# Kernel tuning notes

Hardware: AMD Instinct MI355X
Metric: run time of the kernel (lower is better)

The kernel has to match this reference:

```python
import jax, jax.numpy as jnp
import numpy as np

N_STEPS = 20
ALPHA, BETA = 0.9, 0.8  # synaptic / membrane decay (unused given zero carried state, kept for clarity)


def _lcn_spiking_layer(h, knn, w, b):
    """h: [N, d_in]; knn: [d_out, K] indices into d_in; w: [d_out, K]; b: [1, d_out].
    Gather K neighbors per output node, weight, reduce, then snntorch Synaptic
    update with zero carried state (the source never stores returned syn/mem):
      syn = ALPHA*0 + I = I ; reset = (prev_mem > thr) = 0 ; mem = BETA*0 + syn - 0 = I
    and the layer output is mem (the source keeps the 3rd return value)."""
    g = h[:, knn]                                  # [N, d_out, K] irregular gather
    cur = jnp.sum(g * w[None, :, :], axis=2) + b   # [N, d_out]
    syn = ALPHA * jnp.zeros_like(cur) + cur
    mem = BETA * jnp.zeros_like(cur) + syn         # reset term is zero
    return mem


def setup_inputs() -> dict:
    key = jax.random.key(0)
    B, T, IN_DIM, K, OUT = 32, N_STEPS, 14400, 25, 2
    dims = [7200, 3600, 1800, 900, 450]
    ks = jax.random.split(key, 13)
    inp = {"x": jax.random.normal(ks[0], (B, T, IN_DIM), dtype=jnp.float32)}
    prev = IN_DIM
    for i, d in enumerate(dims):
        inp[f"w{i}"] = jax.random.normal(ks[1 + i], (d, K), dtype=jnp.float32) * (2.0 / K) ** 0.5
        inp[f"b{i}"] = jnp.zeros((1, d), dtype=jnp.float32)
        inp[f"knn{i}"] = jax.random.randint(ks[6 + i], (d, K), 0, prev)
        prev = d
    inp["Wfc"] = jax.random.normal(ks[11], (dims[-1], OUT), dtype=jnp.float32) * (1.0 / dims[-1]) ** 0.5
    inp["bfc"] = jnp.zeros((OUT,), dtype=jnp.float32)
    return inp


def reference(x, w0, w1, w2, w3, w4, b0, b1, b2, b3, b4, Wfc, bfc,
              knn0, knn1, knn2, knn3, knn4):
    # Source loops over 20 timesteps with independent (state never carried) work;
    # fold time into batch to vectorize, then keep the last step's angle only,
    # exactly matching the returned value of the torch forward.
    B, T, D = x.shape
    h = x.reshape(B * T, D)
    layers = ((w0, b0, knn0), (w1, b1, knn1), (w2, b2, knn2), (w3, b3, knn3), (w4, b4, knn4))
    for w, b, knn in layers:
        h = _lcn_spiking_layer(h, knn, w, b)
    angle = h @ Wfc + bfc                     # [B*T, out_dim]
    angle = angle.reshape(B, T, -1)[:, -1]    # last timestep, as in the source
    return angle
```

## Files before the change

kernel.cpp:

```cpp
#include <hip/hip_runtime.h>
#include <hip/hip_bf16.h>


#define ROWS 32
#define TSTEPS 20
#define D0 14400
#define D1 7200
#define D2 3600
#define D3 1800
#define D4 900
#define D5 450
#define KNB 25

template <int DIN, int DOUT, int JPB>
__global__ __launch_bounds__(256)
void layer_lds(const float* __restrict__ hin_base, long long row_stride,
               float* __restrict__ hout,
               const float* __restrict__ w, const float* __restrict__ bvec,
               const int* __restrict__ knn)
{
    __shared__ float s[DIN];
    const int row = blockIdx.y;
    const float* hin = hin_base + (long long)row * row_stride;

    const float4* src = reinterpret_cast<const float4*>(hin);
    float4* dst = reinterpret_cast<float4*>(s);
#pragma unroll 1
    for (int i = threadIdx.x; i < DIN / 4; i += 256)
        dst[i] = src[i];
    __syncthreads();

    const int j0 = blockIdx.x * JPB;
#pragma unroll 1
    for (int j = j0 + threadIdx.x; j < j0 + JPB; j += 256) {
        const int*   kn = knn + j * KNB;
        const float* ww = w   + j * KNB;
        float acc = bvec[j];
#pragma unroll
        for (int k = 0; k < KNB; ++k)
            acc += s[kn[k]] * ww[k];
        hout[row * DOUT + j] = acc;
    }
}

__global__ __launch_bounds__(256)
void lcn_l4_fc(const float* __restrict__ h4,
               const float* __restrict__ w4, const float* __restrict__ b4, const int* __restrict__ knn4,
               const float* __restrict__ Wfc, const float* __restrict__ bfc,
               float* __restrict__ out)
{
    __shared__ float s4[D4];
    __shared__ float s5[D5];

    const int row = blockIdx.x;
    const float* hrow = h4 + row * D4;
    for (int i = threadIdx.x; i < D4; i += 256)
        s4[i] = hrow[i];
    __syncthreads();

    for (int j = threadIdx.x; j < D5; j += 256) {
        const int*   kn = knn4 + j * KNB;
        const float* ww = w4   + j * KNB;
        float acc = b4[j];
#pragma unroll
        for (int k = 0; k < KNB; ++k)
            acc += s4[kn[k]] * ww[k];
        s5[j] = acc;
    }
    __syncthreads();

    const int lane = threadIdx.x & 63;
    const int wid  = threadIdx.x >> 6;
    if (wid < 2) {
        float p = 0.0f;
        for (int i = lane; i < D5; i += 64)
            p += s5[i] * Wfc[i * 2 + wid];
#pragma unroll
        for (int off = 32; off; off >>= 1)
            p += __shfl_down(p, off, 64);
        if (lane == 0)
            out[row * 2 + wid] = p + bfc[wid];
    }
}

extern "C" void kernel_launch(void* const* d_in, const int* in_sizes, int n_in,
                              void* d_out, int out_size, void* d_ws, size_t ws_size,
                              hipStream_t stream)
{
    const float* x    = (const float*)d_in[0];
    const float* w0   = (const float*)d_in[1];
    const float* b0   = (const float*)d_in[2];
    const int*   knn0 = (const int*)  d_in[3];
    const float* w1   = (const float*)d_in[4];
    const float* b1   = (const float*)d_in[5];
    const int*   knn1 = (const int*)  d_in[6];
    const float* w2   = (const float*)d_in[7];
    const float* b2   = (const float*)d_in[8];
    const int*   knn2 = (const int*)  d_in[9];
    const float* w3   = (const float*)d_in[10];
    const float* b3   = (const float*)d_in[11];
    const int*   knn3 = (const int*)  d_in[12];
    const float* w4   = (const float*)d_in[13];
    const float* b4   = (const float*)d_in[14];
    const int*   knn4 = (const int*)  d_in[15];
    const float* Wfc  = (const float*)d_in[16];
    const float* bfc  = (const float*)d_in[17];
    float* out = (float*)d_out;

    float* h1 = (float*)d_ws;
    float* h2 = h1 + ROWS * D1;
    float* h3 = h2 + ROWS * D2;
    float* h4 = h3 + ROWS * D3;

    layer_lds<D0, D1, 900><<<dim3(D1 / 900, ROWS), dim3(256), 0, stream>>>(
        x + (size_t)(TSTEPS - 1) * D0, (long long)TSTEPS * D0, h1, w0, b0, knn0);

    layer_lds<D1, D2, 450><<<dim3(D2 / 450, ROWS), dim3(256), 0, stream>>>(
        h1, D1, h2, w1, b1, knn1);

    layer_lds<D2, D3, 450><<<dim3(D3 / 450, ROWS), dim3(256), 0, stream>>>(
        h2, D2, h3, w2, b2, knn2);

    layer_lds<D3, D4, 225><<<dim3(D4 / 225, ROWS), dim3(256), 0, stream>>>(
        h3, D3, h4, w3, b3, knn3);

    lcn_l4_fc<<<dim3(ROWS), dim3(256), 0, stream>>>(
        h4, w4, b4, knn4, Wfc, bfc, out);
}
```

Before: 132.2 us.

## Transpose intermediate activations to feature-major layout and gather 32 rows per warp

Layers 1-4 now keep activations transposed ([feature][row]), so each half-wavefront gathers the same neighbor index across all 32 rows with coalesced 128-byte loads. This replaces the per-row LDS staging with a single pass per output feature, loading each knn/weight entry once instead of once per row. The last layer and the FC are spread across many blocks and combined with shared and global atomics, which requires a memset of the output and makes float summation order nondeterministic.

New measurement: 128.7 us. 1.03x faster.

```diff
diff --git a/kernel.cpp b/kernel.cpp
--- a/kernel.cpp
+++ b/kernel.cpp
@@ -12,75 +12,91 @@
 #define D5 450
 #define KNB 25
 
-template <int DIN, int DOUT, int JPB>
 __global__ __launch_bounds__(256)
-void layer_lds(const float* __restrict__ hin_base, long long row_stride,
-               float* __restrict__ hout,
-               const float* __restrict__ w, const float* __restrict__ bvec,
-               const int* __restrict__ knn)
+void l0_stage(const float* __restrict__ x, float* __restrict__ h1t,
+              const float* __restrict__ w, const float* __restrict__ bvec,
+              const int* __restrict__ knn)
 {
-    __shared__ float s[DIN];
-    const int row = blockIdx.y;
-    const float* hin = hin_base + (long long)row * row_stride;
+    __shared__ float s[D0];
+    const int r = blockIdx.y;
+    const float* xrow = x + ((size_t)r * TSTEPS + (TSTEPS - 1)) * (size_t)D0;
 
-    const float4* src = reinterpret_cast<const float4*>(hin);
+    const float4* src = reinterpret_cast<const float4*>(xrow);
     float4* dst = reinterpret_cast<float4*>(s);
 #pragma unroll 1
-    for (int i = threadIdx.x; i < DIN / 4; i += 256)
+    for (int i = threadIdx.x; i < D0 / 4; i += 256)
         dst[i] = src[i];
     __syncthreads();
 
-    const int j0 = blockIdx.x * JPB;
+    const int j0 = blockIdx.x * 900;
 #pragma unroll 1
-    for (int j = j0 + threadIdx.x; j < j0 + JPB; j += 256) {
+    for (int j = j0 + threadIdx.x; j < j0 + 900; j += 256) {
         const int*   kn = knn + j * KNB;
         const float* ww = w   + j * KNB;
         float acc = bvec[j];
 #pragma unroll
         for (int k = 0; k < KNB; ++k)
             acc += s[kn[k]] * ww[k];
-        hout[row * DOUT + j] = acc;
+        h1t[(j << 5) + r] = acc;
     }
 }
 
 __global__ __launch_bounds__(256)
-void lcn_l4_fc(const float* __restrict__ h4,
-               const float* __restrict__ w4, const float* __restrict__ b4, const int* __restrict__ knn4,
-               const float* __restrict__ Wfc, const float* __restrict__ bfc,
-               float* __restrict__ out)
+void layer_t_k(const float* __restrict__ pin, float* __restrict__ pout,
+               const float* __restrict__ w, const float* __restrict__ bvec,
+               const int* __restrict__ knn, int npairs)
 {
-    __shared__ float s4[D4];
-    __shared__ float s5[D5];
-
-    const int row = blockIdx.x;
-    const float* hrow = h4 + row * D4;
-    for (int i = threadIdx.x; i < D4; i += 256)
-        s4[i] = hrow[i];
-    __syncthreads();
-
-    for (int j = threadIdx.x; j < D5; j += 256) {
-        const int*   kn = knn4 + j * KNB;
-        const float* ww = w4   + j * KNB;
-        float acc = b4[j];
+    const int lane = threadIdx.x & 63;
+    const int r  = lane & 31;
+    const int jj = lane >> 5;
+    const int nw = gridDim.x << 2;
+#pragma unroll 1
+    for (int jp = (blockIdx.x << 2) + (threadIdx.x >> 6); jp < npairs; jp += nw) {
+        const int j = (jp << 1) + jj;
+        const int*   kn = knn + j * KNB;
+        const float* ww = w   + j * KNB;
+        float acc = bvec[j];
 #pragma unroll
         for (int k = 0; k < KNB; ++k)
-            acc += s4[kn[k]] * ww[k];
-        s5[j] = acc;
+            acc += pin[(kn[k] << 5) + r] * ww[k];
+        pout[(j << 5) + r] = acc;
     }
+}
+
+__global__ __launch_bounds__(256)
+void l4_fc(const float* __restrict__ h4t,
+           const float* __restrict__ w, const float* __restrict__ bvec,
+           const int* __restrict__ knn,
+           const float* __restrict__ Wfc, const float* __restrict__ bfc,
+           float* __restrict__ out)
+{
+    __shared__ float sacc[64];
+    if (threadIdx.x < 64)
+        sacc[threadIdx.x] = (blockIdx.x == 0) ? bfc[threadIdx.x & 1] : 0.0f;
     __syncthreads();
 
     const int lane = threadIdx.x & 63;
-    const int wid  = threadIdx.x >> 6;
-    if (wid < 2) {
-        float p = 0.0f;
-        for (int i = lane; i < D5; i += 64)
-            p += s5[i] * Wfc[i * 2 + wid];
+    const int r  = lane & 31;
+    const int jj = lane >> 5;
+    const int nw = gridDim.x << 2;
+    float c0 = 0.0f, c1 = 0.0f;
+#pragma unroll 1
+    for (int jp = (blockIdx.x << 2) + (threadIdx.x >> 6); jp < D5 / 2; jp += nw) {
+        const int j = (jp << 1) + jj;
+        const int*   kn = knn + j * KNB;
+        const float* ww = w   + j * KNB;
+        float acc = bvec[j];
 #pragma unroll
-        for (int off = 32; off; off >>= 1)
-            p += __shfl_down(p, off, 64);
-        if (lane == 0)
-            out[row * 2 + wid] = p + bfc[wid];
+        for (int k = 0; k < KNB; ++k)
+            acc += h4t[(kn[k] << 5) + r] * ww[k];
+        c0 += acc * Wfc[j * 2 + 0];
+        c1 += acc * Wfc[j * 2 + 1];
     }
+    atomicAdd(&sacc[(r << 1) + 0], c0);
+    atomicAdd(&sacc[(r << 1) + 1], c1);
+    __syncthreads();
+    if (threadIdx.x < 64)
+        atomicAdd(&out[threadIdx.x], sacc[threadIdx.x]);
 }
 
 extern "C" void kernel_launch(void* const* d_in, const int* in_sizes, int n_in,
@@ -107,23 +123,20 @@
     const float* bfc  = (const float*)d_in[17];
     float* out = (float*)d_out;
 
-    float* h1 = (float*)d_ws;
-    float* h2 = h1 + ROWS * D1;
-    float* h3 = h2 + ROWS * D2;
-    float* h4 = h3 + ROWS * D3;
+    float* h1t = (float*)d_ws;
+    float* h2t = h1t + (size_t)D1 * ROWS;
+    float* h3t = h2t + (size_t)D2 * ROWS;
+    float* h4t = h3t + (size_t)D3 * ROWS;
 
-    layer_lds<D0, D1, 900><<<dim3(D1 / 900, ROWS), dim3(256), 0, stream>>>(
-        x + (size_t)(TSTEPS - 1) * D0, (long long)TSTEPS * D0, h1, w0, b0, knn0);
+    hipMemsetAsync(out, 0, (size_t)out_size * sizeof(float), stream);
 
-    layer_lds<D1, D2, 450><<<dim3(D2 / 450, ROWS), dim3(256), 0, stream>>>(
-        h1, D1, h2, w1, b1, knn1);
+    l0_stage<<<dim3(D1 / 900, ROWS), dim3(256), 0, stream>>>(x, h1t, w0, b0, knn0);
 
-    layer_lds<D2, D3, 450><<<dim3(D3 / 450, ROWS), dim3(256), 0, stream>>>(
-        h2, D2, h3, w2, b2, knn2);
+    layer_t_k<<<dim3(450), dim3(256), 0, stream>>>(h1t, h2t, w1, b1, knn1, D2 / 2);
 
-    layer_lds<D3, D4, 225><<<dim3(D4 / 225, ROWS), dim3(256), 0, stream>>>(
-        h3, D3, h4, w3, b3, knn3);
+    layer_t_k<<<dim3(225), dim3(256), 0, stream>>>(h2t, h3t, w2, b2, knn2, D3 / 2);
 
-    lcn_l4_fc<<<dim3(ROWS), dim3(256), 0, stream>>>(
-        h4, w4, b4, knn4, Wfc, bfc, out);
+    layer_t_k<<<dim3(113), dim3(256), 0, stream>>>(h3t, h4t, w3, b3, knn3, D4 / 2);
+
+    l4_fc<<<dim3(57), dim3(256), 0, stream>>>(h4t, w4, b4, knn4, Wfc, bfc, out);
 }
```
